# Performance work log

Measured on AMD Instinct MI355X. Metric: run time of the kernel, lower is better.

The kernel has to match this reference:

```python
import jax, jax.numpy as jnp
import numpy as np

FUTURE_K = 32
NEG_INF = -1e9  # finite large-negative to keep softmax NaN-free on fully-masked rows


def setup_inputs() -> dict:
    key = jax.random.key(0)
    hidden_states = jax.random.normal(key, (4, 2048, 1024), dtype=jnp.float32)
    return {"hidden_states": hidden_states}


def reference(hidden_states) -> jnp.ndarray:
    # Faithful vectorized version of FutureEncoder(summary_method='attention').
    # For each t: window = h[:, t+1 : min(t+1+K, S)], scores = h_t @ window^T,
    # summary_t = softmax(scores) @ window. t = S-1 (empty window) stays zero.
    B, S, D = hidden_states.shape
    offs = jnp.arange(1, FUTURE_K + 1)                 # [K]
    idx = jnp.arange(S)[:, None] + offs[None, :]       # [S, K] future indices t+1..t+K
    valid = idx < S                                     # [S, K]
    idx_c = jnp.minimum(idx, S - 1)
    fw = hidden_states[:, idx_c, :]                     # [B, S, K, D] gathered windows
    scores = jnp.einsum('bsd,bskd->bsk', hidden_states, fw)
    scores = jnp.where(valid[None, :, :], scores, NEG_INF)
    w = jax.nn.softmax(scores, axis=-1)                 # [B, S, K]
    w = jnp.where(valid[None, :, :], w, 0.0)
    out = jnp.einsum('bsk,bskd->bsd', w, fw)            # [B, S, D]
    any_valid = valid.any(axis=-1)                      # [S]; False only at t = S-1
    return jnp.where(any_valid[None, :, None], out, 0.0)
```

## Files before the change

### kernel.cpp

```cpp
#include <hip/hip_runtime.h>
#include <math.h>


constexpr int S_CONST = 2048;
constexpr int D = 1024;
constexpr int G = 16;
constexpr int NTOK = 8192;
constexpr int JW = 48;
constexpr int JP = 49;

typedef short bf16x8 __attribute__((ext_vector_type(8)));
typedef float f32x4  __attribute__((ext_vector_type(4)));

__device__ inline unsigned short f2bf(float x) {
    unsigned u = __builtin_bit_cast(unsigned, x);
    u += 0x7fffu + ((u >> 16) & 1u);
    return (unsigned short)(u >> 16);
}
__device__ inline float bf2f(unsigned short h) {
    unsigned u = ((unsigned)h) << 16;
    return __builtin_bit_cast(float, u);
}

__device__ inline void cvt8(float4 x0, float4 x1, bf16x8& hi, bf16x8& lo) {
    float xs[8] = {x0.x, x0.y, x0.z, x0.w, x1.x, x1.y, x1.z, x1.w};
    #pragma unroll
    for (int e = 0; e < 8; ++e) {
        unsigned short h = f2bf(xs[e]);
        float hf = bf2f(h);
        unsigned short l = f2bf(xs[e] - hf);
        hi[e] = (short)h;
        lo[e] = (short)l;
    }
}

__global__ __launch_bounds__(256)
void convert_kernel(const float* __restrict__ h,
                    short* __restrict__ hh,
                    short* __restrict__ hl) {
    const size_t i = ((size_t)blockIdx.x * 256 + threadIdx.x) * 8;
    float4 x0 = *(const float4*)(h + i);
    float4 x1 = *(const float4*)(h + i + 4);
    bf16x8 vh, vl;
    cvt8(x0, x1, vh, vl);
    *(bf16x8*)(hh + i) = vh;
    *(bf16x8*)(hl + i) = vl;
}

__global__ __launch_bounds__(256, 2)
void future_encoder_pre(const float* __restrict__ h,
                        const short* __restrict__ hh,
                        const short* __restrict__ hl,
                        float* __restrict__ out) {
    __shared__ float sc[4 * G * JP];
    __shared__ float wm[G * JP];

    int bid = blockIdx.x, nblk = gridDim.x, lb = bid;
    if ((nblk & 7) == 0) {
        int per = nblk >> 3;
        lb = (bid & 7) * per + (bid >> 3);
    }

    const int tid  = threadIdx.x;
    const int w    = tid >> 6;
    const int lane = tid & 63;
    const int t0   = lb * G;
    const int s0   = t0 & (S_CONST - 1);
    const int jlim = (S_CONST - 2) - s0;

    {
        const int d0   = w * 256;
        const int mrow = lane & 15;
        const int q8   = (lane >> 4) * 8;

        const size_t abase = (size_t)(t0 + mrow) * D + d0 + q8;
        const short* aph = hh + abase;
        const short* apl = hl + abase;

        int r0 = min(t0 + 1 +  0 + mrow, NTOK - 1);
        int r1 = min(t0 + 1 + 16 + mrow, NTOK - 1);
        int r2 = min(t0 + 1 + 32 + mrow, NTOK - 1);
        const size_t b0 = (size_t)r0 * D + d0 + q8;
        const size_t b1 = (size_t)r1 * D + d0 + q8;
        const size_t b2 = (size_t)r2 * D + d0 + q8;

        f32x4 acc[3] = {{0,0,0,0},{0,0,0,0},{0,0,0,0}};

        #pragma unroll
        for (int kk = 0; kk < 8; ++kk) {
            const int o = kk * 32;
            bf16x8 ah = *(const bf16x8*)(aph + o);
            bf16x8 al = *(const bf16x8*)(apl + o);

            bf16x8 bh = *(const bf16x8*)(hh + b0 + o);
            bf16x8 bl = *(const bf16x8*)(hl + b0 + o);
            acc[0] = __builtin_amdgcn_mfma_f32_16x16x32_bf16(ah, bh, acc[0], 0, 0, 0);
            acc[0] = __builtin_amdgcn_mfma_f32_16x16x32_bf16(ah, bl, acc[0], 0, 0, 0);
            acc[0] = __builtin_amdgcn_mfma_f32_16x16x32_bf16(al, bh, acc[0], 0, 0, 0);

            bh = *(const bf16x8*)(hh + b1 + o);
            bl = *(const bf16x8*)(hl + b1 + o);
            acc[1] = __builtin_amdgcn_mfma_f32_16x16x32_bf16(ah, bh, acc[1], 0, 0, 0);
            acc[1] = __builtin_amdgcn_mfma_f32_16x16x32_bf16(ah, bl, acc[1], 0, 0, 0);
            acc[1] = __builtin_amdgcn_mfma_f32_16x16x32_bf16(al, bh, acc[1], 0, 0, 0);

            bh = *(const bf16x8*)(hh + b2 + o);
            bl = *(const bf16x8*)(hl + b2 + o);
            acc[2] = __builtin_amdgcn_mfma_f32_16x16x32_bf16(ah, bh, acc[2], 0, 0, 0);
            acc[2] = __builtin_amdgcn_mfma_f32_16x16x32_bf16(ah, bl, acc[2], 0, 0, 0);
            acc[2] = __builtin_amdgcn_mfma_f32_16x16x32_bf16(al, bh, acc[2], 0, 0, 0);
        }

        #pragma unroll
        for (int t = 0; t < 3; ++t) {
            #pragma unroll
            for (int r = 0; r < 4; ++r) {
                int m = (lane >> 4) * 4 + r;
                int j = t * 16 + (lane & 15);
                sc[(w * G + m) * JP + j] = acc[t][r];
            }
        }
    }
    __syncthreads();

    {
        const int i   = tid >> 4;
        const int sub = tid & 15;

        float v[3];
        #pragma unroll
        for (int c = 0; c < 3; ++c) {
            int j = sub + c * 16;
            float s = sc[(0 * G + i) * JP + j] + sc[(1 * G + i) * JP + j]
                    + sc[(2 * G + i) * JP + j] + sc[(3 * G + i) * JP + j];
            bool valid = (j >= i) && (j <= i + 31) && (j <= jlim);
            v[c] = valid ? s : -1e9f;
        }
        float mx = fmaxf(v[0], fmaxf(v[1], v[2]));
        #pragma unroll
        for (int d = 1; d < 16; d <<= 1) mx = fmaxf(mx, __shfl_xor(mx, d, 16));

        float e[3];
        float sum = 0.f;
        #pragma unroll
        for (int c = 0; c < 3; ++c) { e[c] = __expf(v[c] - mx); sum += e[c]; }
        #pragma unroll
        for (int d = 1; d < 16; d <<= 1) sum += __shfl_xor(sum, d, 16);

        const bool any = (mx > -5e8f);
        const float inv = any ? (1.0f / sum) : 0.f;
        #pragma unroll
        for (int c = 0; c < 3; ++c) {
            int j = sub + c * 16;
            bool valid = (j >= i) && (j <= i + 31) && (j <= jlim);
            wm[i * JP + j] = valid ? e[c] * inv : 0.f;
        }
    }
    __syncthreads();

    {
        const int i0   = w * 4;
        const int doff = lane * 4;
        const int jhi  = min(min(i0 + 34, JW - 1), jlim);

        float4 a0[4] = {}, a1[4] = {}, a2[4] = {}, a3[4] = {};

        for (int j = i0; j <= jhi; ++j) {
            float w0 = wm[(i0 + 0) * JP + j];
            float w1 = wm[(i0 + 1) * JP + j];
            float w2 = wm[(i0 + 2) * JP + j];
            float w3 = wm[(i0 + 3) * JP + j];
            const float* fp = h + (size_t)(t0 + 1 + j) * D + doff;
            #pragma unroll
            for (int c = 0; c < 4; ++c) {
                float4 f = *(const float4*)(fp + c * 256);
                a0[c].x += w0 * f.x; a0[c].y += w0 * f.y; a0[c].z += w0 * f.z; a0[c].w += w0 * f.w;
                a1[c].x += w1 * f.x; a1[c].y += w1 * f.y; a1[c].z += w1 * f.z; a1[c].w += w1 * f.w;
                a2[c].x += w2 * f.x; a2[c].y += w2 * f.y; a2[c].z += w2 * f.z; a2[c].w += w2 * f.w;
                a3[c].x += w3 * f.x; a3[c].y += w3 * f.y; a3[c].z += w3 * f.z; a3[c].w += w3 * f.w;
            }
        }

        float* o0 = out + (size_t)(t0 + i0) * D + doff;
        #pragma unroll
        for (int c = 0; c < 4; ++c) *(float4*)(o0 + 0 * D + c * 256) = a0[c];
        #pragma unroll
        for (int c = 0; c < 4; ++c) *(float4*)(o0 + 1 * D + c * 256) = a1[c];
        #pragma unroll
        for (int c = 0; c < 4; ++c) *(float4*)(o0 + 2 * D + c * 256) = a2[c];
        #pragma unroll
        for (int c = 0; c < 4; ++c) *(float4*)(o0 + 3 * D + c * 256) = a3[c];
    }
}

__global__ __launch_bounds__(256, 2)
void future_encoder_kernel(const float* __restrict__ h,
                           float* __restrict__ out) {
    __shared__ float sc[4 * G * JP];
    __shared__ float wm[G * JP];

    int bid = blockIdx.x, nblk = gridDim.x, lb = bid;
    if ((nblk & 7) == 0) {
        int per = nblk >> 3;
        lb = (bid & 7) * per + (bid >> 3);
    }

    const int tid  = threadIdx.x;
    const int w    = tid >> 6;
    const int lane = tid & 63;
    const int t0   = lb * G;
    const int s0   = t0 & (S_CONST - 1);
    const int jlim = (S_CONST - 2) - s0;

    {
        const int d0   = w * 256;
        const int mrow = lane & 15;
        const int q8   = (lane >> 4) * 8;

        const float* ap = h + (size_t)(t0 + mrow) * D + d0 + q8;
        const float* bp0; const float* bp1; const float* bp2;
        {
            int r0 = min(t0 + 1 +  0 + mrow, NTOK - 1);
            int r1 = min(t0 + 1 + 16 + mrow, NTOK - 1);
            int r2 = min(t0 + 1 + 32 + mrow, NTOK - 1);
            bp0 = h + (size_t)r0 * D + d0 + q8;
            bp1 = h + (size_t)r1 * D + d0 + q8;
            bp2 = h + (size_t)r2 * D + d0 + q8;
        }

        f32x4 acc[3] = {{0,0,0,0},{0,0,0,0},{0,0,0,0}};

        #pragma unroll
        for (int kk = 0; kk < 8; ++kk) {
            const int o = kk * 32;
            bf16x8 ah, al;
            cvt8(*(const float4*)(ap + o), *(const float4*)(ap + o + 4), ah, al);

            bf16x8 bh, bl;
            cvt8(*(const float4*)(bp0 + o), *(const float4*)(bp0 + o + 4), bh, bl);
            acc[0] = __builtin_amdgcn_mfma_f32_16x16x32_bf16(ah, bh, acc[0], 0, 0, 0);
            acc[0] = __builtin_amdgcn_mfma_f32_16x16x32_bf16(ah, bl, acc[0], 0, 0, 0);
            acc[0] = __builtin_amdgcn_mfma_f32_16x16x32_bf16(al, bh, acc[0], 0, 0, 0);

            cvt8(*(const float4*)(bp1 + o), *(const float4*)(bp1 + o + 4), bh, bl);
            acc[1] = __builtin_amdgcn_mfma_f32_16x16x32_bf16(ah, bh, acc[1], 0, 0, 0);
            acc[1] = __builtin_amdgcn_mfma_f32_16x16x32_bf16(ah, bl, acc[1], 0, 0, 0);
            acc[1] = __builtin_amdgcn_mfma_f32_16x16x32_bf16(al, bh, acc[1], 0, 0, 0);

            cvt8(*(const float4*)(bp2 + o), *(const float4*)(bp2 + o + 4), bh, bl);
            acc[2] = __builtin_amdgcn_mfma_f32_16x16x32_bf16(ah, bh, acc[2], 0, 0, 0);
            acc[2] = __builtin_amdgcn_mfma_f32_16x16x32_bf16(ah, bl, acc[2], 0, 0, 0);
            acc[2] = __builtin_amdgcn_mfma_f32_16x16x32_bf16(al, bh, acc[2], 0, 0, 0);
        }

        #pragma unroll
        for (int t = 0; t < 3; ++t) {
            #pragma unroll
            for (int r = 0; r < 4; ++r) {
                int m = (lane >> 4) * 4 + r;
                int j = t * 16 + (lane & 15);
                sc[(w * G + m) * JP + j] = acc[t][r];
            }
        }
    }
    __syncthreads();

    {
        const int i   = tid >> 4;
        const int sub = tid & 15;

        float v[3];
        #pragma unroll
        for (int c = 0; c < 3; ++c) {
            int j = sub + c * 16;
            float s = sc[(0 * G + i) * JP + j] + sc[(1 * G + i) * JP + j]
                    + sc[(2 * G + i) * JP + j] + sc[(3 * G + i) * JP + j];
            bool valid = (j >= i) && (j <= i + 31) && (j <= jlim);
            v[c] = valid ? s : -1e9f;
        }
        float mx = fmaxf(v[0], fmaxf(v[1], v[2]));
        #pragma unroll
        for (int d = 1; d < 16; d <<= 1) mx = fmaxf(mx, __shfl_xor(mx, d, 16));

        float e[3];
        float sum = 0.f;
        #pragma unroll
        for (int c = 0; c < 3; ++c) { e[c] = __expf(v[c] - mx); sum += e[c]; }
        #pragma unroll
        for (int d = 1; d < 16; d <<= 1) sum += __shfl_xor(sum, d, 16);

        const bool any = (mx > -5e8f);
        const float inv = any ? (1.0f / sum) : 0.f;
        #pragma unroll
        for (int c = 0; c < 3; ++c) {
            int j = sub + c * 16;
            bool valid = (j >= i) && (j <= i + 31) && (j <= jlim);
            wm[i * JP + j] = valid ? e[c] * inv : 0.f;
        }
    }
    __syncthreads();

    {
        const int i0   = w * 4;
        const int doff = lane * 4;
        const int jhi  = min(min(i0 + 34, JW - 1), jlim);

        float4 a0[4] = {}, a1[4] = {}, a2[4] = {}, a3[4] = {};

        for (int j = i0; j <= jhi; ++j) {
            float w0 = wm[(i0 + 0) * JP + j];
            float w1 = wm[(i0 + 1) * JP + j];
            float w2 = wm[(i0 + 2) * JP + j];
            float w3 = wm[(i0 + 3) * JP + j];
            if (w0 + w1 + w2 + w3 != 0.f) {
                const float* fp = h + (size_t)(t0 + 1 + j) * D + doff;
                #pragma unroll
                for (int c = 0; c < 4; ++c) {
                    float4 f = *(const float4*)(fp + c * 256);
                    a0[c].x += w0 * f.x; a0[c].y += w0 * f.y; a0[c].z += w0 * f.z; a0[c].w += w0 * f.w;
                    a1[c].x += w1 * f.x; a1[c].y += w1 * f.y; a1[c].z += w1 * f.z; a1[c].w += w1 * f.w;
                    a2[c].x += w2 * f.x; a2[c].y += w2 * f.y; a2[c].z += w2 * f.z; a2[c].w += w2 * f.w;
                    a3[c].x += w3 * f.x; a3[c].y += w3 * f.y; a3[c].z += w3 * f.z; a3[c].w += w3 * f.w;
                }
            }
        }

        float* o0 = out + (size_t)(t0 + i0) * D + doff;
        #pragma unroll
        for (int c = 0; c < 4; ++c) *(float4*)(o0 + 0 * D + c * 256) = a0[c];
        #pragma unroll
        for (int c = 0; c < 4; ++c) *(float4*)(o0 + 1 * D + c * 256) = a1[c];
        #pragma unroll
        for (int c = 0; c < 4; ++c) *(float4*)(o0 + 2 * D + c * 256) = a2[c];
        #pragma unroll
        for (int c = 0; c < 4; ++c) *(float4*)(o0 + 3 * D + c * 256) = a3[c];
    }
}

extern "C" void kernel_launch(void* const* d_in, const int* in_sizes, int n_in,
                              void* d_out, int out_size, void* d_ws, size_t ws_size,
                              hipStream_t stream) {
    const float* h = (const float*)d_in[0];
    float* out = (float*)d_out;
    const int ntok = in_sizes[0] / D;
    const int blocks = ntok / G;

    const size_t ws_needed = (size_t)NTOK * D * sizeof(short) * 2;
    if (d_ws != nullptr && ws_size >= ws_needed) {
        short* hh = (short*)d_ws;
        short* hl = hh + (size_t)NTOK * D;
        const int cvt_blocks = (ntok * D) / (8 * 256);
        convert_kernel<<<cvt_blocks, 256, 0, stream>>>(h, hh, hl);
        future_encoder_pre<<<blocks, 256, 0, stream>>>(h, hh, hl, out);
    } else {
        future_encoder_kernel<<<blocks, 256, 0, stream>>>(h, out);
    }
}
```

Measured before the change: 124.9 us.

## Interleave bf16 hi/lo planes, double block to 8 waves, prefetch loads

The converter now writes the hi and lo bf16 halves interleaved in one buffer, so each lane loads 16 contiguous values per row with one address stream. The main kernel grows from 4 to 8 waves per block: the score reduction splits D into eight 128-wide slices, and the weighted sum splits D columns across two wave groups. Both the MFMA loop and the PV loop are software-pipelined with register double-buffering of global loads. The aim is more latency hiding and occupancy, at the cost of more shared memory for partial scores and an 8-way reduction in the softmax step.

```diff
diff --git a/kernel.cpp b/kernel.cpp
--- a/kernel.cpp
+++ b/kernel.cpp
@@ -8,6 +8,7 @@
 constexpr int NTOK = 8192;
 constexpr int JW = 48;
 constexpr int JP = 49;
+constexpr int NW = 8;
 
 typedef short bf16x8 __attribute__((ext_vector_type(8)));
 typedef float f32x4  __attribute__((ext_vector_type(4)));
@@ -35,24 +36,21 @@
 }
 
 __global__ __launch_bounds__(256)
-void convert_kernel(const float* __restrict__ h,
-                    short* __restrict__ hh,
-                    short* __restrict__ hl) {
+void convert_kernel(const float* __restrict__ h, short* __restrict__ hp) {
     const size_t i = ((size_t)blockIdx.x * 256 + threadIdx.x) * 8;
     float4 x0 = *(const float4*)(h + i);
     float4 x1 = *(const float4*)(h + i + 4);
     bf16x8 vh, vl;
     cvt8(x0, x1, vh, vl);
-    *(bf16x8*)(hh + i) = vh;
-    *(bf16x8*)(hl + i) = vl;
-}
-
-__global__ __launch_bounds__(256, 2)
+    *(bf16x8*)(hp + i * 2)     = vh;
+    *(bf16x8*)(hp + i * 2 + 8) = vl;
+}
+
+__global__ __launch_bounds__(512, 4)
 void future_encoder_pre(const float* __restrict__ h,
-                        const short* __restrict__ hh,
-                        const short* __restrict__ hl,
+                        const short* __restrict__ hp,
                         float* __restrict__ out) {
-    __shared__ float sc[4 * G * JP];
+    __shared__ float sc[NW * G * JP];
     __shared__ float wm[G * JP];
 
     int bid = blockIdx.x, nblk = gridDim.x, lb = bid;
@@ -69,47 +67,57 @@
     const int jlim = (S_CONST - 2) - s0;
 
     {
-        const int d0   = w * 256;
+        const int d0   = w * 128;
         const int mrow = lane & 15;
         const int q8   = (lane >> 4) * 8;
-
-        const size_t abase = (size_t)(t0 + mrow) * D + d0 + q8;
-        const short* aph = hh + abase;
-        const short* apl = hl + abase;
-
-        int r0 = min(t0 + 1 +  0 + mrow, NTOK - 1);
-        int r1 = min(t0 + 1 + 16 + mrow, NTOK - 1);
-        int r2 = min(t0 + 1 + 32 + mrow, NTOK - 1);
-        const size_t b0 = (size_t)r0 * D + d0 + q8;
-        const size_t b1 = (size_t)r1 * D + d0 + q8;
-        const size_t b2 = (size_t)r2 * D + d0 + q8;
+        const int dof  = d0 * 2 + q8 * 2;
+
+        const short* A = hp + (size_t)(t0 + mrow) * 2048 + dof;
+        int r0 = min(t0 +  1 + mrow, NTOK - 1);
+        int r1 = min(t0 + 17 + mrow, NTOK - 1);
+        int r2 = min(t0 + 33 + mrow, NTOK - 1);
+        const short* B0 = hp + (size_t)r0 * 2048 + dof;
+        const short* B1 = hp + (size_t)r1 * 2048 + dof;
+        const short* B2 = hp + (size_t)r2 * 2048 + dof;
 
         f32x4 acc[3] = {{0,0,0,0},{0,0,0,0},{0,0,0,0}};
 
-        #pragma unroll
-        for (int kk = 0; kk < 8; ++kk) {
-            const int o = kk * 32;
-            bf16x8 ah = *(const bf16x8*)(aph + o);
-            bf16x8 al = *(const bf16x8*)(apl + o);
-
-            bf16x8 bh = *(const bf16x8*)(hh + b0 + o);
-            bf16x8 bl = *(const bf16x8*)(hl + b0 + o);
-            acc[0] = __builtin_amdgcn_mfma_f32_16x16x32_bf16(ah, bh, acc[0], 0, 0, 0);
-            acc[0] = __builtin_amdgcn_mfma_f32_16x16x32_bf16(ah, bl, acc[0], 0, 0, 0);
-            acc[0] = __builtin_amdgcn_mfma_f32_16x16x32_bf16(al, bh, acc[0], 0, 0, 0);
-
-            bh = *(const bf16x8*)(hh + b1 + o);
-            bl = *(const bf16x8*)(hl + b1 + o);
-            acc[1] = __builtin_amdgcn_mfma_f32_16x16x32_bf16(ah, bh, acc[1], 0, 0, 0);
-            acc[1] = __builtin_amdgcn_mfma_f32_16x16x32_bf16(ah, bl, acc[1], 0, 0, 0);
-            acc[1] = __builtin_amdgcn_mfma_f32_16x16x32_bf16(al, bh, acc[1], 0, 0, 0);
-
-            bh = *(const bf16x8*)(hh + b2 + o);
-            bl = *(const bf16x8*)(hl + b2 + o);
-            acc[2] = __builtin_amdgcn_mfma_f32_16x16x32_bf16(ah, bh, acc[2], 0, 0, 0);
-            acc[2] = __builtin_amdgcn_mfma_f32_16x16x32_bf16(ah, bl, acc[2], 0, 0, 0);
-            acc[2] = __builtin_amdgcn_mfma_f32_16x16x32_bf16(al, bh, acc[2], 0, 0, 0);
-        }
+        #define LD8(p, o) (*(const bf16x8*)((p) + (o)))
+        bf16x8 cah = LD8(A,0),  cal = LD8(A,8);
+        bf16x8 c0h = LD8(B0,0), c0l = LD8(B0,8);
+        bf16x8 c1h = LD8(B1,0), c1l = LD8(B1,8);
+        bf16x8 c2h = LD8(B2,0), c2l = LD8(B2,8);
+
+        #pragma unroll
+        for (int kk = 0; kk < 4; ++kk) {
+            bf16x8 nah, nal, n0h, n0l, n1h, n1l, n2h, n2l;
+            if (kk < 3) {
+                const int o = (kk + 1) * 64;
+                nah = LD8(A,o);  nal = LD8(A,o+8);
+                n0h = LD8(B0,o); n0l = LD8(B0,o+8);
+                n1h = LD8(B1,o); n1l = LD8(B1,o+8);
+                n2h = LD8(B2,o); n2l = LD8(B2,o+8);
+            }
+            acc[0] = __builtin_amdgcn_mfma_f32_16x16x32_bf16(cah, c0h, acc[0], 0, 0, 0);
+            acc[0] = __builtin_amdgcn_mfma_f32_16x16x32_bf16(cah, c0l, acc[0], 0, 0, 0);
+            acc[0] = __builtin_amdgcn_mfma_f32_16x16x32_bf16(cal, c0h, acc[0], 0, 0, 0);
+
+            acc[1] = __builtin_amdgcn_mfma_f32_16x16x32_bf16(cah, c1h, acc[1], 0, 0, 0);
+            acc[1] = __builtin_amdgcn_mfma_f32_16x16x32_bf16(cah, c1l, acc[1], 0, 0, 0);
+            acc[1] = __builtin_amdgcn_mfma_f32_16x16x32_bf16(cal, c1h, acc[1], 0, 0, 0);
+
+            acc[2] = __builtin_amdgcn_mfma_f32_16x16x32_bf16(cah, c2h, acc[2], 0, 0, 0);
+            acc[2] = __builtin_amdgcn_mfma_f32_16x16x32_bf16(cah, c2l, acc[2], 0, 0, 0);
+            acc[2] = __builtin_amdgcn_mfma_f32_16x16x32_bf16(cal, c2h, acc[2], 0, 0, 0);
+
+            if (kk < 3) {
+                cah = nah; cal = nal;
+                c0h = n0h; c0l = n0l;
+                c1h = n1h; c1l = n1l;
+                c2h = n2h; c2l = n2l;
+            }
+        }
+        #undef LD8
 
         #pragma unroll
         for (int t = 0; t < 3; ++t) {
@@ -123,7 +131,7 @@
     }
     __syncthreads();
 
-    {
+    if (tid < 256) {
         const int i   = tid >> 4;
         const int sub = tid & 15;
 
@@ -131,8 +139,10 @@
         #pragma unroll
         for (int c = 0; c < 3; ++c) {
             int j = sub + c * 16;
-            float s = sc[(0 * G + i) * JP + j] + sc[(1 * G + i) * JP + j]
-                    + sc[(2 * G + i) * JP + j] + sc[(3 * G + i) * JP + j];
+            float s = 0.f;
+            #pragma unroll
+            for (int ww = 0; ww < NW; ++ww)
+                s += sc[(ww * G + i) * JP + j];
             bool valid = (j >= i) && (j <= i + 31) && (j <= jlim);
             v[c] = valid ? s : -1e9f;
         }
@@ -159,37 +169,51 @@
     __syncthreads();
 
     {
-        const int i0   = w * 4;
-        const int doff = lane * 4;
+        const int i0   = (w & 3) * 4;
+        const int cc   = (w >> 2) * 2;
+        const int doff = cc * 256 + lane * 4;
         const int jhi  = min(min(i0 + 34, JW - 1), jlim);
 
-        float4 a0[4] = {}, a1[4] = {}, a2[4] = {}, a3[4] = {};
-
-        for (int j = i0; j <= jhi; ++j) {
-            float w0 = wm[(i0 + 0) * JP + j];
-            float w1 = wm[(i0 + 1) * JP + j];
-            float w2 = wm[(i0 + 2) * JP + j];
-            float w3 = wm[(i0 + 3) * JP + j];
-            const float* fp = h + (size_t)(t0 + 1 + j) * D + doff;
-            #pragma unroll
-            for (int c = 0; c < 4; ++c) {
-                float4 f = *(const float4*)(fp + c * 256);
-                a0[c].x += w0 * f.x; a0[c].y += w0 * f.y; a0[c].z += w0 * f.z; a0[c].w += w0 * f.w;
-                a1[c].x += w1 * f.x; a1[c].y += w1 * f.y; a1[c].z += w1 * f.z; a1[c].w += w1 * f.w;
-                a2[c].x += w2 * f.x; a2[c].y += w2 * f.y; a2[c].z += w2 * f.z; a2[c].w += w2 * f.w;
-                a3[c].x += w3 * f.x; a3[c].y += w3 * f.y; a3[c].z += w3 * f.z; a3[c].w += w3 * f.w;
-            }
-        }
+        float4 a0[2] = {}, a1[2] = {}, a2[2] = {}, a3[2] = {};
+
+        const float* fp0 = h + (size_t)(t0 + 1 + i0) * D + doff;
+        float4 fa = *(const float4*)(fp0);
+        float4 fb = *(const float4*)(fp0 + 256);
+
+        #define PVFMA(j_) do {                                                  \
+            float w0 = wm[(i0 + 0) * JP + (j_)];                                \
+            float w1 = wm[(i0 + 1) * JP + (j_)];                                \
+            float w2 = wm[(i0 + 2) * JP + (j_)];                                \
+            float w3 = wm[(i0 + 3) * JP + (j_)];                                \
+            a0[0].x += w0 * fa.x; a0[0].y += w0 * fa.y; a0[0].z += w0 * fa.z; a0[0].w += w0 * fa.w; \
+            a1[0].x += w1 * fa.x; a1[0].y += w1 * fa.y; a1[0].z += w1 * fa.z; a1[0].w += w1 * fa.w; \
+            a2[0].x += w2 * fa.x; a2[0].y += w2 * fa.y; a2[0].z += w2 * fa.z; a2[0].w += w2 * fa.w; \
+            a3[0].x += w3 * fa.x; a3[0].y += w3 * fa.y; a3[0].z += w3 * fa.z; a3[0].w += w3 * fa.w; \
+            a0[1].x += w0 * fb.x; a0[1].y += w0 * fb.y; a0[1].z += w0 * fb.z; a0[1].w += w0 * fb.w; \
+            a1[1].x += w1 * fb.x; a1[1].y += w1 * fb.y; a1[1].z += w1 * fb.z; a1[1].w += w1 * fb.w; \
+            a2[1].x += w2 * fb.x; a2[1].y += w2 * fb.y; a2[1].z += w2 * fb.z; a2[1].w += w2 * fb.w; \
+            a3[1].x += w3 * fb.x; a3[1].y += w3 * fb.y; a3[1].z += w3 * fb.z; a3[1].w += w3 * fb.w; \
+        } while (0)
+
+        for (int j = i0; j < jhi; ++j) {
+            const float* fn = h + (size_t)(t0 + 2 + j) * D + doff;
+            float4 na = *(const float4*)(fn);
+            float4 nb = *(const float4*)(fn + 256);
+            PVFMA(j);
+            fa = na; fb = nb;
+        }
+        PVFMA(jhi);
+        #undef PVFMA
 
         float* o0 = out + (size_t)(t0 + i0) * D + doff;
-        #pragma unroll
-        for (int c = 0; c < 4; ++c) *(float4*)(o0 + 0 * D + c * 256) = a0[c];
-        #pragma unroll
-        for (int c = 0; c < 4; ++c) *(float4*)(o0 + 1 * D + c * 256) = a1[c];
-        #pragma unroll
-        for (int c = 0; c < 4; ++c) *(float4*)(o0 + 2 * D + c * 256) = a2[c];
-        #pragma unroll
-        for (int c = 0; c < 4; ++c) *(float4*)(o0 + 3 * D + c * 256) = a3[c];
+        *(float4*)(o0 + 0 * D)       = a0[0];
+        *(float4*)(o0 + 0 * D + 256) = a0[1];
+        *(float4*)(o0 + 1 * D)       = a1[0];
+        *(float4*)(o0 + 1 * D + 256) = a1[1];
+        *(float4*)(o0 + 2 * D)       = a2[0];
+        *(float4*)(o0 + 2 * D + 256) = a2[1];
+        *(float4*)(o0 + 3 * D)       = a3[0];
+        *(float4*)(o0 + 3 * D + 256) = a3[1];
     }
 }
 
@@ -347,11 +371,10 @@
 
     const size_t ws_needed = (size_t)NTOK * D * sizeof(short) * 2;
     if (d_ws != nullptr && ws_size >= ws_needed) {
-        short* hh = (short*)d_ws;
-        short* hl = hh + (size_t)NTOK * D;
+        short* hp = (short*)d_ws;
         const int cvt_blocks = (ntok * D) / (8 * 256);
-        convert_kernel<<<cvt_blocks, 256, 0, stream>>>(h, hh, hl);
-        future_encoder_pre<<<blocks, 256, 0, stream>>>(h, hh, hl, out);
+        convert_kernel<<<cvt_blocks, 256, 0, stream>>>(h, hp);
+        future_encoder_pre<<<blocks, 512, 0, stream>>>(h, hp, out);
     } else {
         future_encoder_kernel<<<blocks, 256, 0, stream>>>(h, out);
     }
```

Measured after the change: 116.2 us. 7.0% less time.
